# Optimization experiments

Measured on AMD Instinct MI355X. Metric: run time of the kernel, lower is better.

The kernel has to match this reference:

```python
import jax, jax.numpy as jnp
import numpy as np

H = 512
N = 512
BSZ = 8
L = 4096
DIRECTION = 2  # 0=forward, 1=backward, 2=bidirectional (split N in half)


def setup_inputs() -> dict:
    key = jax.random.key(0)
    k = jax.random.split(key, 6)
    u = jax.random.normal(k[0], (BSZ, L, H), jnp.float32)
    # variable lengths in [L//2, L]
    lengths = jax.random.randint(k[1], (BSZ,), L // 2, L + 1).astype(jnp.int32)
    # LRU init: r_min=0, r_max=1, max_phase=2*pi
    u1 = jax.random.uniform(k[2], (N,), jnp.float32)
    nu_log = jnp.log(-0.5 * jnp.log(u1))
    u2 = jax.random.uniform(k[3], (N,), jnp.float32)
    theta_log = jnp.log(2.0 * np.pi * u2)
    lam = jnp.exp(-jnp.exp(nu_log) + 1j * jnp.exp(theta_log))  # (N,) complex
    gamma = jnp.sqrt(1.0 - jnp.abs(lam) ** 2)[:, None]          # (N,1)
    B = jax.random.normal(k[4], (H, N, 2), jnp.float32) / np.float32(np.sqrt(2 * H)) * gamma
    C = jax.random.normal(k[5], (2, H, N), jnp.float32) / np.float32(np.sqrt(N))
    return {"u": u, "lengths": lengths, "nu_log": nu_log, "theta_log": theta_log, "B": B, "C": C}


def _lru_scan(lam, Bu, reverse):
    """Diagonal linear recurrence x_t = lam * x_{t-1} + Bu_t along axis 2 via associative scan.
    lam: (n,) complex; Bu: (B, n, L) complex."""
    a = jnp.broadcast_to(lam[None, :, None], Bu.shape)

    def op(e1, e2):
        a1, b1 = e1
        a2, b2 = e2
        return a1 * a2, a2 * b1 + b2

    _, x = jax.lax.associative_scan(op, (a, Bu), axis=2, reverse=reverse)
    return x


def reference(u, lengths, nu_log, theta_log, B, C):
    lam = jnp.exp(-jnp.exp(nu_log) + 1j * jnp.exp(theta_log))  # (N,)
    Bc = B[..., 0] + 1j * B[..., 1]                            # (H, N) complex
    Bu = jnp.einsum('blh,hn->bnl', u, Bc)                      # (B, N, L) complex
    mask = jnp.arange(L)[None, :] < lengths[:, None]           # (B, L)
    Bu = Bu * mask[:, None, :]
    if DIRECTION == 2:
        h = N // 2
        x = jnp.concatenate([
            _lru_scan(lam[:h], Bu[:, :h], reverse=False),
            _lru_scan(lam[h:], Bu[:, h:], reverse=True),
        ], axis=1)
    elif DIRECTION == 0:
        x = _lru_scan(lam, Bu, reverse=False)
    else:
        x = _lru_scan(lam, Bu, reverse=True)
    x = x * mask[:, None, :]           # zero outputs past each sequence length
    x = jnp.swapaxes(x, 1, 2)          # (B, L, N)
    y = x.real @ C[0] - x.imag @ C[1]  # (B, L, H)  (requires H == N, as in source)
    return y
```

## Files before the change

kernel.cpp:

```cpp
#include <hip/hip_runtime.h>

#define L_SEQ   4096
#define BSZQ    8
#define ROWS    (BSZQ * L_SEQ)
#define KC1     512
#define NC1     1024
#define KC2     1024
#define NC2     512
#define CHUNK   64
#define NCHUNK  64

typedef __attribute__((ext_vector_type(8))) short bfrag;
typedef __attribute__((ext_vector_type(4))) float ffrag;

static __device__ __forceinline__ unsigned short f2bf(float f) {
    union { float f; unsigned int u; } v; v.f = f;
    unsigned int r = v.u + 0x7fffu + ((v.u >> 16) & 1u);
    return (unsigned short)(r >> 16);
}
static __device__ __forceinline__ unsigned int pk2(float a, float b) {
    return (unsigned int)f2bf(a) | ((unsigned int)f2bf(b) << 16);
}
static __device__ __forceinline__ float2 unpk2(unsigned int u) {
    union { unsigned int u; float f; } a, b;
    a.u = u << 16;
    b.u = u & 0xffff0000u;
    return make_float2(a.f, b.f);
}

static __device__ __forceinline__ void async16(const void* g, void* l) {
    __builtin_amdgcn_global_load_lds(
        (const __attribute__((address_space(1))) unsigned int*)g,
        (__attribute__((address_space(3))) unsigned int*)l,
        16, 0, 0);
}

__global__ __launch_bounds__(256) void prep_conv_kernel(
    const float* __restrict__ u, const int* __restrict__ lengths,
    const float* __restrict__ B, const float* __restrict__ C,
    const float* __restrict__ nu_log, const float* __restrict__ theta_log,
    unsigned short* __restrict__ ub, unsigned short* __restrict__ Bt,
    unsigned short* __restrict__ Dt, float2* __restrict__ lam)
{
    int g = blockIdx.x, tid = threadIdx.x;
    if (g < 8192) {
        int idx = g * 256 + tid;
        int row = idx >> 6;
        int l = row & (L_SEQ - 1), b = row >> 12;
        bool keep = (l < lengths[b]);
        union { unsigned int s[4]; float4 f; } o;
        if (keep) {
            const float4 a = *(const float4*)(u + (size_t)idx * 8);
            const float4 c = *(const float4*)(u + (size_t)idx * 8 + 4);
            o.s[0] = pk2(a.x, a.y); o.s[1] = pk2(a.z, a.w);
            o.s[2] = pk2(c.x, c.y); o.s[3] = pk2(c.z, c.w);
        } else {
            o.s[0] = o.s[1] = o.s[2] = o.s[3] = 0u;
        }
        *(float4*)(ub + (size_t)idx * 8) = o.f;
    } else if (g < 10240) {
        int idx = (g - 8192) * 256 + tid;
        int n2 = idx >> 9, h = idx & 511;
        Bt[idx] = f2bf(B[(size_t)h * 1024 + n2]);
    } else if (g < 12288) {
        int idx = (g - 10240) * 256 + tid;
        int j = idx >> 10, k = idx & 1023;
        int n = k >> 1, c = k & 1;
        float v = C[((size_t)c * 512 + n) * 512 + j];
        Dt[idx] = f2bf(c ? -v : v);
    } else {
#pragma unroll
        for (int r = 0; r < 2; r++) {
            int n = tid + r * 256;
            float mag = expf(-expf(nu_log[n]));
            float th  = expf(theta_log[n]);
            lam[n] = make_float2(mag * cosf(th), mag * sinf(th));
        }
    }
}

template<int KD, int ND, bool BF16OUT>
__global__ __launch_bounds__(256, 4) void gemm_db(
    const unsigned short* __restrict__ A,
    const unsigned short* __restrict__ Bt,
    void* __restrict__ Co)
{
    __shared__ __align__(16) unsigned short As[2][128 * 32];
    __shared__ __align__(16) unsigned short Bs[2][128 * 32];

    const int tid  = threadIdx.x;
    const int lane = tid & 63, w = tid >> 6;
    const int q = lane >> 4, m16 = lane & 15;
    const int wr = (w >> 1) * 64, wc = (w & 1) * 64;
    const int row0 = blockIdx.x * 128;
    const int col0 = blockIdx.y * 128;

    ffrag acc[4][4];
#pragma unroll
    for (int i = 0; i < 4; i++)
#pragma unroll
        for (int j = 0; j < 4; j++) acc[i][j] = (ffrag)0.f;

#define STAGE_T(GP, TB, KT, GR0) do {                                          \
    _Pragma("unroll")                                                          \
    for (int j_ = 0; j_ < 2; j_++) {                                           \
        int s_ = j_ * 256 + tid;                                               \
        int r_ = s_ >> 2;                                                      \
        int cs_ = (s_ & 3) ^ ((r_ >> 1) & 3);                                  \
        async16(GP + (size_t)((GR0) + r_) * KD + (KT) + cs_ * 8,               \
                &TB[(size_t)(j_ * 256 + w * 64) * 8]);                         \
    }                                                                          \
} while (0)

    STAGE_T(A,  As[0], 0, row0);
    STAGE_T(Bt, Bs[0], 0, col0);
    __syncthreads();

    int c = 0;
    for (int kt = 0; kt < KD; kt += 32) {
        if (kt + 32 < KD) {
            STAGE_T(A,  As[c ^ 1], kt + 32, row0);
            STAGE_T(Bt, Bs[c ^ 1], kt + 32, col0);
        }
        bfrag a[4], b[4];
#pragma unroll
        for (int ri = 0; ri < 4; ri++) {
            int r_ = wr + ri * 16 + m16;
            a[ri] = *(const bfrag*)&As[c][r_ * 32 + (q ^ ((r_ >> 1) & 3)) * 8];
        }
#pragma unroll
        for (int ci = 0; ci < 4; ci++) {
            int r_ = wc + ci * 16 + m16;
            b[ci] = *(const bfrag*)&Bs[c][r_ * 32 + (q ^ ((r_ >> 1) & 3)) * 8];
        }
#pragma unroll
        for (int ri = 0; ri < 4; ri++)
#pragma unroll
            for (int ci = 0; ci < 4; ci++)
                acc[ri][ci] = __builtin_amdgcn_mfma_f32_16x16x32_bf16(
                    a[ri], b[ci], acc[ri][ci], 0, 0, 0);
        __syncthreads();
        c ^= 1;
    }
#undef STAGE_T

    if (BF16OUT) {
        unsigned int* Cb = (unsigned int*)Co;
        const int colc0 = (col0 >> 1) + (w & 1) * 32;
#pragma unroll
        for (int ri = 0; ri < 4; ri++)
#pragma unroll
            for (int cp = 0; cp < 2; cp++)
#pragma unroll
                for (int r4 = 0; r4 < 4; r4++) {
                    float a0 = acc[ri][cp * 2][r4];
                    float a1 = acc[ri][cp * 2 + 1][r4];
                    float b0 = __shfl_xor(a0, 1);
                    float b1 = __shfl_xor(a1, 1);
                    unsigned int uo = (m16 & 1) ? pk2(b1, a1) : pk2(a0, b0);
                    int row = row0 + wr + ri * 16 + q * 4 + r4;
                    int ccol = (cp * 2 + (m16 & 1)) * 8 + (m16 >> 1);
                    Cb[(size_t)row * (ND / 2) + colc0 + ccol] = uo;
                }
    } else {
        float* Cf = (float*)Co;
#pragma unroll
        for (int ri = 0; ri < 4; ri++)
#pragma unroll
            for (int r4 = 0; r4 < 4; r4++) {
                int row = row0 + wr + ri * 16 + q * 4 + r4;
#pragma unroll
                for (int ci = 0; ci < 4; ci++) {
                    int col = col0 + wc + ci * 16 + m16;
                    Cf[(size_t)row * ND + col] = acc[ri][ci][r4];
                }
            }
    }
}

__global__ __launch_bounds__(256) void scan_states_kernel(
    const unsigned int* __restrict__ bu, const float2* __restrict__ lam,
    float2* __restrict__ states)
{
    int t = threadIdx.x;
    int b = blockIdx.x >> 6;
    int c = blockIdx.x & 63;
    float4 lm = *(const float4*)&lam[2 * t];
    float x0r = 0.f, x0i = 0.f, x1r = 0.f, x1i = 0.f;
    bool fwd = (t < 128);
    int l0 = fwd ? (c * CHUNK) : (c * CHUNK + CHUNK - 1);
    const unsigned int* p = bu + ((size_t)b * L_SEQ + l0) * 512 + 2 * t;
    ptrdiff_t step = fwd ? 512 : -512;
#pragma unroll 8
    for (int i = 0; i < CHUNK; i++) {
        uint2 v = *(const uint2*)p;
        float2 v0 = unpk2(v.x), v1 = unpk2(v.y);
        float n0r = lm.x * x0r - lm.y * x0i + v0.x;
        float n0i = lm.x * x0i + lm.y * x0r + v0.y;
        float n1r = lm.z * x1r - lm.w * x1i + v1.x;
        float n1i = lm.z * x1i + lm.w * x1r + v1.y;
        x0r = n0r; x0i = n0i; x1r = n1r; x1i = n1i;
        p += step;
    }
    *(float4*)&states[((size_t)b * NCHUNK + c) * 512 + 2 * t] =
        make_float4(x0r, x0i, x1r, x1i);
}

__global__ __launch_bounds__(64) void scan_combine_kernel(
    const float2* __restrict__ states, float2* __restrict__ carries,
    const float2* __restrict__ lam)
{
    int b = blockIdx.x >> 2;
    int s = blockIdx.x & 3;
    int np = s * 64 + threadIdx.x;
    int n0 = 2 * np;
    bool fwd = (s < 2);
    float4 lm = *(const float4*)&lam[n0];

    float a0r = lm.x, a0i = lm.y, a1r = lm.z, a1i = lm.w;
#pragma unroll
    for (int i = 0; i < 6; i++) {
        float n0r_ = a0r * a0r - a0i * a0i; a0i = 2.f * a0r * a0i; a0r = n0r_;
        float n1r_ = a1r * a1r - a1i * a1i; a1i = 2.f * a1r * a1i; a1r = n1r_;
    }

    float c0r = 0.f, c0i = 0.f, c1r = 0.f, c1i = 0.f;
    for (int g = 0; g < 8; ++g) {
        float4 st[8];
#pragma unroll
        for (int k = 0; k < 8; ++k) {
            int cc = fwd ? (g * 8 + k) : (63 - (g * 8 + k));
            st[k] = *(const float4*)&states[((size_t)b * NCHUNK + cc) * 512 + n0];
        }
#pragma unroll
        for (int k = 0; k < 8; ++k) {
            int cc = fwd ? (g * 8 + k) : (63 - (g * 8 + k));
            *(float4*)&carries[((size_t)b * NCHUNK + cc) * 512 + n0] =
                make_float4(c0r, c0i, c1r, c1i);
            float n0r_ = a0r * c0r - a0i * c0i + st[k].x;
            float n0i_ = a0r * c0i + a0i * c0r + st[k].y;
            float n1r_ = a1r * c1r - a1i * c1i + st[k].z;
            float n1i_ = a1r * c1i + a1i * c1r + st[k].w;
            c0r = n0r_; c0i = n0i_; c1r = n1r_; c1i = n1i_;
        }
    }
}

__global__ __launch_bounds__(256) void scan_apply_kernel(
    unsigned int* __restrict__ bu, const float2* __restrict__ carries,
    const float2* __restrict__ lam, const int* __restrict__ lengths)
{
    int t = threadIdx.x;
    int b = blockIdx.x >> 6;
    int c = blockIdx.x & 63;
    int len = lengths[b];
    float4 lm = *(const float4*)&lam[2 * t];
    float4 cy = *(const float4*)&carries[((size_t)b * NCHUNK + c) * 512 + 2 * t];
    bool fwd = (t < 128);
    int l0 = fwd ? (c * CHUNK) : (c * CHUNK + CHUNK - 1);
    int dl = fwd ? 1 : -1;
    unsigned int* p = bu + ((size_t)b * L_SEQ + l0) * 512 + 2 * t;
    ptrdiff_t step = fwd ? 512 : -512;
    float x0r = cy.x, x0i = cy.y, x1r = cy.z, x1i = cy.w;
    int l = l0;
#pragma unroll 8
    for (int i = 0; i < CHUNK; i++) {
        uint2 v = *(const uint2*)p;
        float2 v0 = unpk2(v.x), v1 = unpk2(v.y);
        float n0r = lm.x * x0r - lm.y * x0i + v0.x;
        float n0i = lm.x * x0i + lm.y * x0r + v0.y;
        float n1r = lm.z * x1r - lm.w * x1i + v1.x;
        float n1i = lm.z * x1i + lm.w * x1r + v1.y;
        x0r = n0r; x0i = n0i; x1r = n1r; x1i = n1i;
        uint2 o2;
        o2.x = (l >= len) ? 0u : pk2(x0r, x0i);
        o2.y = (l >= len) ? 0u : pk2(x1r, x1i);
        *(uint2*)p = o2;
        p += step; l += dl;
    }
}

extern "C" void kernel_launch(void* const* d_in, const int* in_sizes, int n_in,
                              void* d_out, int out_size, void* d_ws, size_t ws_size,
                              hipStream_t stream)
{
    const float* u        = (const float*)d_in[0];
    const int*   lengths  = (const int*)  d_in[1];
    const float* nu_log   = (const float*)d_in[2];
    const float* theta_log= (const float*)d_in[3];
    const float* B        = (const float*)d_in[4];
    const float* C        = (const float*)d_in[5];
    float* y = (float*)d_out;

    char* wp = (char*)d_ws;
    float2* lam     = (float2*)wp;  wp += 4096;
    float2* states  = (float2*)wp;  wp += (size_t)BSZQ * NCHUNK * 512 * 8;
    float2* carries = (float2*)wp;  wp += (size_t)BSZQ * NCHUNK * 512 * 8;
    unsigned int* bu = (unsigned int*)wp; wp += (size_t)ROWS * 512 * 4;
    unsigned short* ub = (unsigned short*)wp; wp += (size_t)ROWS * 512 * 2;
    unsigned short* Bt = (unsigned short*)wp; wp += (size_t)NC1 * KC1 * 2;
    unsigned short* Dt = (unsigned short*)wp; wp += (size_t)NC2 * KC2 * 2;

    prep_conv_kernel<<<12289, 256, 0, stream>>>(
        u, lengths, B, C, nu_log, theta_log, ub, Bt, Dt, lam);

    {
        dim3 grid(ROWS / 128, NC1 / 128);
        gemm_db<KC1, NC1, true><<<grid, 256, 0, stream>>>(ub, Bt, bu);
    }

    scan_states_kernel<<<BSZQ * NCHUNK, 256, 0, stream>>>(bu, lam, states);
    scan_combine_kernel<<<BSZQ * 4, 64, 0, stream>>>(states, carries, lam);
    scan_apply_kernel<<<BSZQ * NCHUNK, 256, 0, stream>>>(bu, carries, lam, lengths);

    {
        dim3 grid(ROWS / 128, NC2 / 128);
        gemm_db<KC2, NC2, false><<<grid, 256, 0, stream>>>(
            (const unsigned short*)bu, Dt, y);
    }
}
```

Before: 263.1 us.

## Fuse chunk-state reduction of the LRU scan into the first GEMM epilogue

Removes the separate scan_states kernel. The first GEMM's bf16-output epilogue now computes each 64-row chunk's end state directly from the accumulator registers. It does this as a weighted sum with powers of lambda, reduced across lanes with shuffles. This avoids re-reading the full bu tensor from memory and one kernel launch. The trade-offs are extra complex arithmetic and register pressure in the epilogue, and the chunk states are now formed from fp32 accumulators rather than the bf16-rounded values.

```diff
diff --git a/kernel.cpp b/kernel.cpp
--- a/kernel.cpp
+++ b/kernel.cpp
@@ -26,6 +26,9 @@
     a.u = u << 16;
     b.u = u & 0xffff0000u;
     return make_float2(a.f, b.f);
+}
+static __device__ __forceinline__ float2 cmul(float2 a, float2 b) {
+    return make_float2(a.x * b.x - a.y * b.y, a.x * b.y + a.y * b.x);
 }
 
 static __device__ __forceinline__ void async16(const void* g, void* l) {
@@ -83,7 +86,9 @@
 __global__ __launch_bounds__(256, 4) void gemm_db(
     const unsigned short* __restrict__ A,
     const unsigned short* __restrict__ Bt,
-    void* __restrict__ Co)
+    void* __restrict__ Co,
+    const float2* __restrict__ lamg,
+    float2* __restrict__ states)
 {
     __shared__ __align__(16) unsigned short As[2][128 * 32];
     __shared__ __align__(16) unsigned short Bs[2][128 * 32];
@@ -147,10 +152,24 @@
     if (BF16OUT) {
         unsigned int* Cb = (unsigned int*)Co;
         const int colc0 = (col0 >> 1) + (w & 1) * 32;
-#pragma unroll
-        for (int ri = 0; ri < 4; ri++)
-#pragma unroll
-            for (int cp = 0; cp < 2; cp++)
+        const bool fwd = (col0 * 2 < ND);
+        const int b_  = row0 >> 12;
+        const int cch = ((row0 >> 6) & 63) + (wr >> 6);
+        const float2 one = make_float2(1.f, 0.f);
+        float2 Ssum[2];
+#pragma unroll
+        for (int cp = 0; cp < 2; cp++) {
+            const int ccol = (cp * 2 + (m16 & 1)) * 8 + (m16 >> 1);
+            float2 lm  = lamg[colc0 + ccol];
+            float2 c2  = cmul(lm, lm),  c3  = cmul(c2, lm);
+            float2 p4  = cmul(c2, c2),  p8  = cmul(p4, p4), p12 = cmul(p8, p4);
+            float2 a16 = cmul(p8, p8),  a32 = cmul(a16, a16), a48 = cmul(a32, a16);
+            int eq = fwd ? 3 - q : q;
+            float2 Bq = (eq == 0) ? one : (eq == 1) ? p4 : (eq == 2) ? p8 : p12;
+            float2 S = make_float2(0.f, 0.f);
+#pragma unroll
+            for (int ri = 0; ri < 4; ri++) {
+                float2 T = make_float2(0.f, 0.f);
 #pragma unroll
                 for (int r4 = 0; r4 < 4; r4++) {
                     float a0 = acc[ri][cp * 2][r4];
@@ -159,9 +178,41 @@
                     float b1 = __shfl_xor(a1, 1);
                     unsigned int uo = (m16 & 1) ? pk2(b1, a1) : pk2(a0, b0);
                     int row = row0 + wr + ri * 16 + q * 4 + r4;
-                    int ccol = (cp * 2 + (m16 & 1)) * 8 + (m16 >> 1);
                     Cb[(size_t)row * (ND / 2) + colc0 + ccol] = uo;
+                    float2 v = (m16 & 1) ? make_float2(b1, a1)
+                                         : make_float2(a0, b0);
+                    float2 wv = fwd ? ((r4 == 3) ? one : (r4 == 2) ? lm
+                                      : (r4 == 1) ? c2 : c3)
+                                    : ((r4 == 0) ? one : (r4 == 1) ? lm
+                                      : (r4 == 2) ? c2 : c3);
+                    T.x += wv.x * v.x - wv.y * v.y;
+                    T.y += wv.x * v.y + wv.y * v.x;
                 }
+                float2 wa = fwd ? ((ri == 3) ? one : (ri == 2) ? a16
+                                  : (ri == 1) ? a32 : a48)
+                                : ((ri == 0) ? one : (ri == 1) ? a16
+                                  : (ri == 2) ? a32 : a48);
+                float2 E = cmul(wa, Bq);
+                S.x += E.x * T.x - E.y * T.y;
+                S.y += E.x * T.y + E.y * T.x;
+            }
+            Ssum[cp] = S;
+        }
+#pragma unroll
+        for (int cp = 0; cp < 2; cp++) {
+            Ssum[cp].x += __shfl_xor(Ssum[cp].x, 16);
+            Ssum[cp].y += __shfl_xor(Ssum[cp].y, 16);
+            Ssum[cp].x += __shfl_xor(Ssum[cp].x, 32);
+            Ssum[cp].y += __shfl_xor(Ssum[cp].y, 32);
+        }
+        if (q == 0) {
+#pragma unroll
+            for (int cp = 0; cp < 2; cp++) {
+                int ccol = (cp * 2 + (m16 & 1)) * 8 + (m16 >> 1);
+                states[((size_t)b_ * NCHUNK + cch) * 512 + colc0 + ccol] =
+                    Ssum[cp];
+            }
+        }
     } else {
         float* Cf = (float*)Co;
 #pragma unroll
@@ -176,34 +227,6 @@
                 }
             }
     }
-}
-
-__global__ __launch_bounds__(256) void scan_states_kernel(
-    const unsigned int* __restrict__ bu, const float2* __restrict__ lam,
-    float2* __restrict__ states)
-{
-    int t = threadIdx.x;
-    int b = blockIdx.x >> 6;
-    int c = blockIdx.x & 63;
-    float4 lm = *(const float4*)&lam[2 * t];
-    float x0r = 0.f, x0i = 0.f, x1r = 0.f, x1i = 0.f;
-    bool fwd = (t < 128);
-    int l0 = fwd ? (c * CHUNK) : (c * CHUNK + CHUNK - 1);
-    const unsigned int* p = bu + ((size_t)b * L_SEQ + l0) * 512 + 2 * t;
-    ptrdiff_t step = fwd ? 512 : -512;
-#pragma unroll 8
-    for (int i = 0; i < CHUNK; i++) {
-        uint2 v = *(const uint2*)p;
-        float2 v0 = unpk2(v.x), v1 = unpk2(v.y);
-        float n0r = lm.x * x0r - lm.y * x0i + v0.x;
-        float n0i = lm.x * x0i + lm.y * x0r + v0.y;
-        float n1r = lm.z * x1r - lm.w * x1i + v1.x;
-        float n1i = lm.z * x1i + lm.w * x1r + v1.y;
-        x0r = n0r; x0i = n0i; x1r = n1r; x1i = n1i;
-        p += step;
-    }
-    *(float4*)&states[((size_t)b * NCHUNK + c) * 512 + 2 * t] =
-        make_float4(x0r, x0i, x1r, x1i);
 }
 
 __global__ __launch_bounds__(64) void scan_combine_kernel(
@@ -306,16 +329,16 @@
 
     {
         dim3 grid(ROWS / 128, NC1 / 128);
-        gemm_db<KC1, NC1, true><<<grid, 256, 0, stream>>>(ub, Bt, bu);
-    }
-
-    scan_states_kernel<<<BSZQ * NCHUNK, 256, 0, stream>>>(bu, lam, states);
+        gemm_db<KC1, NC1, true><<<grid, 256, 0, stream>>>(
+            ub, Bt, bu, lam, states);
+    }
+
     scan_combine_kernel<<<BSZQ * 4, 64, 0, stream>>>(states, carries, lam);
     scan_apply_kernel<<<BSZQ * NCHUNK, 256, 0, stream>>>(bu, carries, lam, lengths);
 
     {
         dim3 grid(ROWS / 128, NC2 / 128);
         gemm_db<KC2, NC2, false><<<grid, 256, 0, stream>>>(
-            (const unsigned short*)bu, Dt, y);
-    }
-}
+            (const unsigned short*)bu, Dt, y, nullptr, nullptr);
+    }
+}
```

New measurement: 256.0 us. -2.7%, faster.
